# Kernel tuning notes

Hardware: AMD Instinct MI355X
Metric: run time of the kernel (lower is better)

## Reference

```python
import jax, jax.numpy as jnp
import numpy as np

N_SLICES = 2  # init kwarg n_slices


def affine_grid_3d(theta, D, H, W):
    """torch.nn.functional.affine_grid for 5D output, align_corners=False.
    theta: [B,3,4]; returns grid [B,D,H,W,3] with last dim (x,y,z) ~ (W,H,D)."""
    xs = (jnp.arange(W, dtype=theta.dtype) + 0.5) * (2.0 / W) - 1.0
    ys = (jnp.arange(H, dtype=theta.dtype) + 0.5) * (2.0 / H) - 1.0
    zs = (jnp.arange(D, dtype=theta.dtype) + 0.5) * (2.0 / D) - 1.0
    zz, yy, xx = jnp.meshgrid(zs, ys, xs, indexing='ij')
    base = jnp.stack([xx, yy, zz, jnp.ones_like(xx)], axis=-1)  # [D,H,W,4]
    return jnp.einsum('bij,dhwj->bdhwi', theta, base)  # [B,D,H,W,3]


def grid_sample_3d_zeros(vol, grid):
    """torch.nn.functional.grid_sample, mode='bilinear' (trilinear for 5D),
    padding_mode='zeros', align_corners=False.
    vol: [B,C,D,H,W]; grid: [B,D,H,W,3] normalized xyz coords."""
    B, C, D, H, W = vol.shape
    ix = ((grid[..., 0] + 1.0) * W - 1.0) * 0.5
    iy = ((grid[..., 1] + 1.0) * H - 1.0) * 0.5
    iz = ((grid[..., 2] + 1.0) * D - 1.0) * 0.5
    ix0 = jnp.floor(ix); iy0 = jnp.floor(iy); iz0 = jnp.floor(iz)
    fx = ix - ix0; fy = iy - iy0; fz = iz - iz0

    def gather(v, z, y, x):  # v: [C,D,H,W], idx: [D,H,W] -> [C,D,H,W]
        return v[:, z, y, x]

    out = jnp.zeros((B, C, D, H, W), vol.dtype)
    for dz in (0, 1):
        for dy in (0, 1):
            for dx in (0, 1):
                xi = ix0 + dx; yi = iy0 + dy; zi = iz0 + dz
                w = (jnp.where(dx, fx, 1.0 - fx)
                     * jnp.where(dy, fy, 1.0 - fy)
                     * jnp.where(dz, fz, 1.0 - fz))
                valid = ((xi >= 0) & (xi < W) & (yi >= 0) & (yi < H)
                         & (zi >= 0) & (zi < D))
                xc = jnp.clip(xi, 0, W - 1).astype(jnp.int32)
                yc = jnp.clip(yi, 0, H - 1).astype(jnp.int32)
                zc = jnp.clip(zi, 0, D - 1).astype(jnp.int32)
                vals = jax.vmap(gather)(vol, zc, yc, xc)  # [B,C,D,H,W]
                out = out + vals * (w * valid)[:, None]
    return out


def skip_connector(x, b_grid_affines):
    B, C, SPAT, _ = x.shape
    # zero volume with the 2D slice stack placed at the central W-plane
    vol = jnp.zeros((B, C, SPAT, SPAT, SPAT), x.dtype).at[..., SPAT // 2].set(x)
    chunks = jnp.split(vol, N_SLICES, axis=1)
    outs = []
    for i in range(N_SLICES):
        aff = b_grid_affines[i].astype(jnp.float32)  # [B,4,4]
        # get_zooms: column norms of rotation block
        zooms = jnp.sqrt((aff[:, :3, :3] ** 2).sum(axis=1))  # [B,3]
        # rescale_rot_components_with_diag(aff, 1/zooms) == aff @ diag(1/zx,1/zy,1/zz,1)
        scale = jnp.concatenate([1.0 / zooms, jnp.ones((aff.shape[0], 1), aff.dtype)], axis=1)
        aff = aff * scale[:, None, :]
        theta = jnp.linalg.inv(aff)[:, :3, :]  # [B,3,4]
        grid = affine_grid_3d(theta, SPAT, SPAT, SPAT)
        outs.append(grid_sample_3d_zeros(chunks[i], grid))
    return jnp.concatenate(outs, axis=1)  # [B,C,SPAT,SPAT,SPAT]


def setup_inputs() -> dict:
    key = jax.random.key(0)
    k1, k2 = jax.random.split(key)
    B, C, SPAT = 2, 32, 96
    x = jax.random.normal(k1, (B, C, SPAT, SPAT), dtype=jnp.float32)
    # near-identity invertible homogeneous affines for the two views (SA, HLA)
    noise = 0.1 * jax.random.normal(k2, (2, B, 4, 4), dtype=jnp.float32)
    aff = jnp.eye(4, dtype=jnp.float32)[None, None] + noise
    aff = aff.at[..., 3, :].set(jnp.array([0.0, 0.0, 0.0, 1.0], dtype=jnp.float32))
    return {"x": x, "b_grid_affines": aff}


def reference(x, b_grid_affines):
    return skip_connector(x, b_grid_affines)
```

## Files before the change

### kernel.cpp

```cpp
#include <hip/hip_runtime.h>
#include <math.h>

#define SPAT 96
#define PLANE (SPAT*SPAT*SPAT)
#define IMG   (SPAT*SPAT)

__device__ inline void invert4(const float m[16], float inv[16]) {
    inv[0]  =  m[5]*m[10]*m[15] - m[5]*m[11]*m[14] - m[9]*m[6]*m[15] + m[9]*m[7]*m[14] + m[13]*m[6]*m[11] - m[13]*m[7]*m[10];
    inv[4]  = -m[4]*m[10]*m[15] + m[4]*m[11]*m[14] + m[8]*m[6]*m[15] - m[8]*m[7]*m[14] - m[12]*m[6]*m[11] + m[12]*m[7]*m[10];
    inv[8]  =  m[4]*m[9]*m[15]  - m[4]*m[11]*m[13] - m[8]*m[5]*m[15] + m[8]*m[7]*m[13] + m[12]*m[5]*m[11] - m[12]*m[7]*m[9];
    inv[12] = -m[4]*m[9]*m[14]  + m[4]*m[10]*m[13] + m[8]*m[5]*m[14] - m[8]*m[6]*m[13] - m[12]*m[5]*m[10] + m[12]*m[6]*m[9];
    inv[1]  = -m[1]*m[10]*m[15] + m[1]*m[11]*m[14] + m[9]*m[2]*m[15] - m[9]*m[3]*m[14] - m[13]*m[2]*m[11] + m[13]*m[3]*m[10];
    inv[5]  =  m[0]*m[10]*m[15] - m[0]*m[11]*m[14] - m[8]*m[2]*m[15] + m[8]*m[3]*m[14] + m[12]*m[2]*m[11] - m[12]*m[3]*m[10];
    inv[9]  = -m[0]*m[9]*m[15]  + m[0]*m[11]*m[13] + m[8]*m[1]*m[15] - m[8]*m[3]*m[13] - m[12]*m[1]*m[11] + m[12]*m[3]*m[9];
    inv[13] =  m[0]*m[9]*m[14]  - m[0]*m[10]*m[13] - m[8]*m[1]*m[14] + m[8]*m[2]*m[13] + m[12]*m[1]*m[10] - m[12]*m[2]*m[9];
    inv[2]  =  m[1]*m[6]*m[15]  - m[1]*m[7]*m[14]  - m[5]*m[2]*m[15] + m[5]*m[3]*m[14] + m[13]*m[2]*m[7]  - m[13]*m[3]*m[6];
    inv[6]  = -m[0]*m[6]*m[15]  + m[0]*m[7]*m[14]  + m[4]*m[2]*m[15] - m[4]*m[3]*m[14] - m[12]*m[2]*m[7]  + m[12]*m[3]*m[6];
    inv[10] =  m[0]*m[5]*m[15]  - m[0]*m[7]*m[13]  - m[4]*m[1]*m[15] + m[4]*m[3]*m[13] + m[12]*m[1]*m[7]  - m[12]*m[3]*m[5];
    inv[14] = -m[0]*m[5]*m[14]  + m[0]*m[6]*m[13]  + m[4]*m[1]*m[14] - m[4]*m[2]*m[13] - m[12]*m[1]*m[6]  + m[12]*m[2]*m[5];
    inv[3]  = -m[1]*m[6]*m[11]  + m[1]*m[7]*m[10]  + m[5]*m[2]*m[11] - m[5]*m[3]*m[10] - m[9]*m[2]*m[7]   + m[9]*m[3]*m[6];
    inv[7]  =  m[0]*m[6]*m[11]  - m[0]*m[7]*m[10]  - m[4]*m[2]*m[11] + m[4]*m[3]*m[10] + m[8]*m[2]*m[7]   - m[8]*m[3]*m[6];
    inv[11] = -m[0]*m[5]*m[11]  + m[0]*m[7]*m[9]   + m[4]*m[1]*m[11] - m[4]*m[3]*m[9]  - m[8]*m[1]*m[7]   + m[8]*m[3]*m[5];
    inv[15] =  m[0]*m[5]*m[10]  - m[0]*m[6]*m[9]   - m[4]*m[1]*m[10] + m[4]*m[2]*m[9]  + m[8]*m[1]*m[6]   - m[8]*m[2]*m[5];
    float det  = m[0]*inv[0] + m[1]*inv[4] + m[2]*inv[8] + m[3]*inv[12];
    float rdet = 1.0f / det;
    for (int i = 0; i < 16; ++i) inv[i] *= rdet;
}

__global__ void prep_kernel(const float* __restrict__ aff_in,
                            float* __restrict__ Mout) {
    int t = threadIdx.x;
    if (t >= 4) return;
    float A[16];
    #pragma unroll
    for (int i = 0; i < 16; ++i) A[i] = aff_in[t * 16 + i];
    #pragma unroll
    for (int j = 0; j < 3; ++j) {
        float z = sqrtf(A[0*4+j]*A[0*4+j] + A[1*4+j]*A[1*4+j] + A[2*4+j]*A[2*4+j]);
        float rz = 1.0f / z;
        #pragma unroll
        for (int i = 0; i < 4; ++i) A[i*4+j] *= rz;
    }
    float inv[16];
    invert4(A, inv);
    float* M = Mout + t * 12;
    #pragma unroll
    for (int r = 0; r < 3; ++r) {
        float T0 = inv[r*4+0], T1 = inv[r*4+1], T2 = inv[r*4+2], T3 = inv[r*4+3];
        M[r*4+0] = T0;
        M[r*4+1] = T1;
        M[r*4+2] = T2;
        M[r*4+3] = -47.5f * (T0 + T1 + T2) + 48.0f * T3 + 47.5f;
    }
}

__global__ __launch_bounds__(256) void sample_kernel(
        const float* __restrict__ xin,
        const float* __restrict__ Mw,
        float* __restrict__ out) {
    int tf = blockIdx.x * 256 + threadIdx.x;
    int w4 = tf % 24;
    int h  = tf / 24;
    int d  = blockIdx.y;
    int sb = blockIdx.z;
    int s  = sb >> 1;
    int b  = sb & 1;

    const float* M = Mw + sb * 12;
    float Mxw = M[0], Mxh = M[1], Mxd = M[2],  Mx0 = M[3];
    float Myw = M[4], Myh = M[5], Myd = M[6],  My0 = M[7];
    float Mzw = M[8], Mzh = M[9], Mzd = M[10], Mz0 = M[11];

    float fh = (float)h, fd = (float)d;
    float bx = Mxh * fh + Mxd * fd + Mx0;
    float by = Myh * fh + Myd * fd + My0;
    float bz = Mzh * fh + Mzd * fd + Mz0;

    int w0 = w4 * 4;
    float wgt[4][4];
    int   off[4][4];
    bool  any = false;

    #pragma unroll
    for (int j = 0; j < 4; ++j) {
        float fw = (float)(w0 + j);
        float ix = Mxw * fw + bx;
        float iy = Myw * fw + by;
        float iz = Mzw * fw + bz;
        float wx = 1.0f - fabsf(ix - 48.0f);

        float w00 = 0.f, w01 = 0.f, w10 = 0.f, w11 = 0.f;
        int   o00 = 0,   o01 = 0,   o10 = 0,   o11 = 0;
        if (wx > 0.0f) {
            any = true;
            float yf = floorf(iy), zf = floorf(iz);
            float fy = iy - yf,    fz = iz - zf;
            int y0 = (int)yf, z0 = (int)zf;
            bool vy0 = (y0 >= 0)  & (y0 <  SPAT);
            bool vy1 = (y0 >= -1) & (y0 <  SPAT - 1);
            bool vz0 = (z0 >= 0)  & (z0 <  SPAT);
            bool vz1 = (z0 >= -1) & (z0 <  SPAT - 1);
            int y0c = min(max(y0, 0),     SPAT - 1);
            int y1c = min(max(y0 + 1, 0), SPAT - 1);
            int z0c = min(max(z0, 0),     SPAT - 1);
            int z1c = min(max(z0 + 1, 0), SPAT - 1);
            float wy0 = 1.0f - fy, wy1 = fy;
            float wz0 = 1.0f - fz, wz1 = fz;
            w00 = wx * wz0 * wy0 * ((vz0 & vy0) ? 1.0f : 0.0f);
            w01 = wx * wz0 * wy1 * ((vz0 & vy1) ? 1.0f : 0.0f);
            w10 = wx * wz1 * wy0 * ((vz1 & vy0) ? 1.0f : 0.0f);
            w11 = wx * wz1 * wy1 * ((vz1 & vy1) ? 1.0f : 0.0f);
            o00 = z0c * SPAT + y0c;  o01 = z0c * SPAT + y1c;
            o10 = z1c * SPAT + y0c;  o11 = z1c * SPAT + y1c;
        }
        wgt[j][0] = w00; wgt[j][1] = w01; wgt[j][2] = w10; wgt[j][3] = w11;
        off[j][0] = o00; off[j][1] = o01; off[j][2] = o10; off[j][3] = o11;
    }

    size_t cbase = (size_t)(b * 32 + s * 16);
    float* op = out + cbase * (size_t)PLANE + ((size_t)d * SPAT + h) * SPAT + w0;

    if (!any) {
        float4 z4 = make_float4(0.f, 0.f, 0.f, 0.f);
        #pragma unroll
        for (int c = 0; c < 16; ++c)
            *reinterpret_cast<float4*>(op + (size_t)c * PLANE) = z4;
    } else {
        const float* img = xin + cbase * (size_t)IMG;
        #pragma unroll
        for (int c = 0; c < 16; ++c) {
            const float* ic = img + (size_t)c * IMG;
            float r[4];
            #pragma unroll
            for (int j = 0; j < 4; ++j) {
                r[j] = wgt[j][0] * ic[off[j][0]] + wgt[j][1] * ic[off[j][1]]
                     + wgt[j][2] * ic[off[j][2]] + wgt[j][3] * ic[off[j][3]];
            }
            *reinterpret_cast<float4*>(op + (size_t)c * PLANE) =
                make_float4(r[0], r[1], r[2], r[3]);
        }
    }
}

extern "C" void kernel_launch(void* const* d_in, const int* in_sizes, int n_in,
                              void* d_out, int out_size, void* d_ws, size_t ws_size,
                              hipStream_t stream) {
    const float* x   = (const float*)d_in[0];
    const float* aff = (const float*)d_in[1];
    float* out = (float*)d_out;
    float* M   = (float*)d_ws;

    prep_kernel<<<1, 64, 0, stream>>>(aff, M);

    dim3 grid(9, SPAT, 4);
    sample_kernel<<<grid, 256, 0, stream>>>(x, M, out);
}
```

Baseline: 257.7 us.

## Zero output with bulk memset kernel and sample only the nonzero slab per row

A grid-stride zero kernel now clears the whole output. A new slab kernel then handles each (d,h) row and a group of 4 channels, solving analytically for the w-range where the x-tent weight is nonzero and writing only those voxels. The matrix prep moves into the slab kernel, computed by thread 0 into shared memory, which removes the separate prep launch. The cost is that every output byte is written once by the memset and the slab is written again, and the slab stores become scalar, strided across threads by row, instead of coalesced float4 stores.

```diff
diff --git a/kernel.cpp b/kernel.cpp
--- a/kernel.cpp
+++ b/kernel.cpp
@@ -4,6 +4,7 @@
 #define SPAT 96
 #define PLANE (SPAT*SPAT*SPAT)
 #define IMG   (SPAT*SPAT)
+#define OUT_FLOATS (64 * PLANE)
 
 __device__ inline void invert4(const float m[16], float inv[16]) {
     inv[0]  =  m[5]*m[10]*m[15] - m[5]*m[11]*m[14] - m[9]*m[6]*m[15] + m[9]*m[7]*m[14] + m[13]*m[6]*m[11] - m[13]*m[7]*m[10];
@@ -27,117 +28,115 @@
     for (int i = 0; i < 16; ++i) inv[i] *= rdet;
 }
 
-__global__ void prep_kernel(const float* __restrict__ aff_in,
-                            float* __restrict__ Mout) {
-    int t = threadIdx.x;
-    if (t >= 4) return;
-    float A[16];
-    #pragma unroll
-    for (int i = 0; i < 16; ++i) A[i] = aff_in[t * 16 + i];
-    #pragma unroll
-    for (int j = 0; j < 3; ++j) {
-        float z = sqrtf(A[0*4+j]*A[0*4+j] + A[1*4+j]*A[1*4+j] + A[2*4+j]*A[2*4+j]);
-        float rz = 1.0f / z;
-        #pragma unroll
-        for (int i = 0; i < 4; ++i) A[i*4+j] *= rz;
-    }
-    float inv[16];
-    invert4(A, inv);
-    float* M = Mout + t * 12;
-    #pragma unroll
-    for (int r = 0; r < 3; ++r) {
-        float T0 = inv[r*4+0], T1 = inv[r*4+1], T2 = inv[r*4+2], T3 = inv[r*4+3];
-        M[r*4+0] = T0;
-        M[r*4+1] = T1;
-        M[r*4+2] = T2;
-        M[r*4+3] = -47.5f * (T0 + T1 + T2) + 48.0f * T3 + 47.5f;
-    }
+__global__ __launch_bounds__(256) void zero_kernel(float4* __restrict__ out) {
+    const size_t n4 = OUT_FLOATS / 4;
+    size_t i = (size_t)blockIdx.x * 256 + threadIdx.x;
+    size_t stride = (size_t)gridDim.x * 256;
+    float4 z = make_float4(0.f, 0.f, 0.f, 0.f);
+    for (; i < n4; i += stride) out[i] = z;
 }
 
-__global__ __launch_bounds__(256) void sample_kernel(
+__global__ __launch_bounds__(256) void slab_kernel(
         const float* __restrict__ xin,
-        const float* __restrict__ Mw,
+        const float* __restrict__ aff_in,
         float* __restrict__ out) {
-    int tf = blockIdx.x * 256 + threadIdx.x;
-    int w4 = tf % 24;
-    int h  = tf / 24;
-    int d  = blockIdx.y;
-    int sb = blockIdx.z;
+    __shared__ float Ms[12];
+    int sb = blockIdx.y;
+    if (threadIdx.x == 0) {
+        float A[16];
+        #pragma unroll
+        for (int i = 0; i < 16; ++i) A[i] = aff_in[sb * 16 + i];
+        #pragma unroll
+        for (int j = 0; j < 3; ++j) {
+            float z = sqrtf(A[0*4+j]*A[0*4+j] + A[1*4+j]*A[1*4+j] + A[2*4+j]*A[2*4+j]);
+            float rz = 1.0f / z;
+            #pragma unroll
+            for (int i = 0; i < 4; ++i) A[i*4+j] *= rz;
+        }
+        float inv[16];
+        invert4(A, inv);
+        #pragma unroll
+        for (int r = 0; r < 3; ++r) {
+            float T0 = inv[r*4+0], T1 = inv[r*4+1], T2 = inv[r*4+2], T3 = inv[r*4+3];
+            Ms[r*4+0] = T0;
+            Ms[r*4+1] = T1;
+            Ms[r*4+2] = T2;
+            Ms[r*4+3] = -47.5f * (T0 + T1 + T2) + 48.0f * T3 + 47.5f;
+        }
+    }
+    __syncthreads();
+
+    int t  = blockIdx.x * 256 + threadIdx.x;
+    int cg = t & 3;
+    int hd = t >> 2;
+    int h  = hd % SPAT;
+    int d  = hd / SPAT;
     int s  = sb >> 1;
     int b  = sb & 1;
 
-    const float* M = Mw + sb * 12;
-    float Mxw = M[0], Mxh = M[1], Mxd = M[2],  Mx0 = M[3];
-    float Myw = M[4], Myh = M[5], Myd = M[6],  My0 = M[7];
-    float Mzw = M[8], Mzh = M[9], Mzd = M[10], Mz0 = M[11];
+    float Mxw = Ms[0], Mxh = Ms[1], Mxd = Ms[2],  Mx0 = Ms[3];
+    float Myw = Ms[4], Myh = Ms[5], Myd = Ms[6],  My0 = Ms[7];
+    float Mzw = Ms[8], Mzh = Ms[9], Mzd = Ms[10], Mz0 = Ms[11];
 
     float fh = (float)h, fd = (float)d;
     float bx = Mxh * fh + Mxd * fd + Mx0;
     float by = Myh * fh + Myd * fd + My0;
     float bz = Mzh * fh + Mzd * fd + Mz0;
 
-    int w0 = w4 * 4;
-    float wgt[4][4];
-    int   off[4][4];
-    bool  any = false;
+    int wlo, whi;
+    if (fabsf(Mxw) > 1e-6f) {
+        float w1 = (47.0f - bx) / Mxw;
+        float w2 = (49.0f - bx) / Mxw;
+        float wmin = fminf(w1, w2), wmax = fmaxf(w1, w2);
+        wlo = (int)ceilf(wmin);
+        whi = (int)floorf(wmax);
+        wlo = max(wlo, 0);
+        whi = min(whi, SPAT - 1);
+    } else {
+        bool in = fabsf(bx - 48.0f) < 1.0f;
+        wlo = in ? 0 : 1;
+        whi = in ? SPAT - 1 : 0;
+    }
+    if (wlo > whi) return;
 
-    #pragma unroll
-    for (int j = 0; j < 4; ++j) {
-        float fw = (float)(w0 + j);
+    size_t cbase = (size_t)(b * 32 + s * 16 + cg * 4);
+    const float* img = xin + cbase * (size_t)IMG;
+    float* op = out + cbase * (size_t)PLANE + ((size_t)d * SPAT + h) * SPAT;
+
+    for (int w = wlo; w <= whi; ++w) {
+        float fw = (float)w;
         float ix = Mxw * fw + bx;
+        float wx = 1.0f - fabsf(ix - 48.0f);
+        if (wx <= 0.0f) continue;
         float iy = Myw * fw + by;
         float iz = Mzw * fw + bz;
-        float wx = 1.0f - fabsf(ix - 48.0f);
 
-        float w00 = 0.f, w01 = 0.f, w10 = 0.f, w11 = 0.f;
-        int   o00 = 0,   o01 = 0,   o10 = 0,   o11 = 0;
-        if (wx > 0.0f) {
-            any = true;
-            float yf = floorf(iy), zf = floorf(iz);
-            float fy = iy - yf,    fz = iz - zf;
-            int y0 = (int)yf, z0 = (int)zf;
-            bool vy0 = (y0 >= 0)  & (y0 <  SPAT);
-            bool vy1 = (y0 >= -1) & (y0 <  SPAT - 1);
-            bool vz0 = (z0 >= 0)  & (z0 <  SPAT);
-            bool vz1 = (z0 >= -1) & (z0 <  SPAT - 1);
-            int y0c = min(max(y0, 0),     SPAT - 1);
-            int y1c = min(max(y0 + 1, 0), SPAT - 1);
-            int z0c = min(max(z0, 0),     SPAT - 1);
-            int z1c = min(max(z0 + 1, 0), SPAT - 1);
-            float wy0 = 1.0f - fy, wy1 = fy;
-            float wz0 = 1.0f - fz, wz1 = fz;
-            w00 = wx * wz0 * wy0 * ((vz0 & vy0) ? 1.0f : 0.0f);
-            w01 = wx * wz0 * wy1 * ((vz0 & vy1) ? 1.0f : 0.0f);
-            w10 = wx * wz1 * wy0 * ((vz1 & vy0) ? 1.0f : 0.0f);
-            w11 = wx * wz1 * wy1 * ((vz1 & vy1) ? 1.0f : 0.0f);
-            o00 = z0c * SPAT + y0c;  o01 = z0c * SPAT + y1c;
-            o10 = z1c * SPAT + y0c;  o11 = z1c * SPAT + y1c;
-        }
-        wgt[j][0] = w00; wgt[j][1] = w01; wgt[j][2] = w10; wgt[j][3] = w11;
-        off[j][0] = o00; off[j][1] = o01; off[j][2] = o10; off[j][3] = o11;
-    }
+        float yf = floorf(iy), zf = floorf(iz);
+        float fy = iy - yf,    fz = iz - zf;
+        int y0 = (int)yf, z0 = (int)zf;
+        bool vy0 = (y0 >= 0)  & (y0 <  SPAT);
+        bool vy1 = (y0 >= -1) & (y0 <  SPAT - 1);
+        bool vz0 = (z0 >= 0)  & (z0 <  SPAT);
+        bool vz1 = (z0 >= -1) & (z0 <  SPAT - 1);
+        int y0c = min(max(y0, 0),     SPAT - 1);
+        int y1c = min(max(y0 + 1, 0), SPAT - 1);
+        int z0c = min(max(z0, 0),     SPAT - 1);
+        int z1c = min(max(z0 + 1, 0), SPAT - 1);
+        float wy0 = 1.0f - fy, wy1 = fy;
+        float wz0 = 1.0f - fz, wz1 = fz;
+        float w00 = wx * wz0 * wy0 * ((vz0 & vy0) ? 1.0f : 0.0f);
+        float w01 = wx * wz0 * wy1 * ((vz0 & vy1) ? 1.0f : 0.0f);
+        float w10 = wx * wz1 * wy0 * ((vz1 & vy0) ? 1.0f : 0.0f);
+        float w11 = wx * wz1 * wy1 * ((vz1 & vy1) ? 1.0f : 0.0f);
+        int o00 = z0c * SPAT + y0c, o01 = z0c * SPAT + y1c;
+        int o10 = z1c * SPAT + y0c, o11 = z1c * SPAT + y1c;
 
-    size_t cbase = (size_t)(b * 32 + s * 16);
-    float* op = out + cbase * (size_t)PLANE + ((size_t)d * SPAT + h) * SPAT + w0;
-
-    if (!any) {
-        float4 z4 = make_float4(0.f, 0.f, 0.f, 0.f);
         #pragma unroll
-        for (int c = 0; c < 16; ++c)
-            *reinterpret_cast<float4*>(op + (size_t)c * PLANE) = z4;
-    } else {
-        const float* img = xin + cbase * (size_t)IMG;
-        #pragma unroll
-        for (int c = 0; c < 16; ++c) {
+        for (int c = 0; c < 4; ++c) {
             const float* ic = img + (size_t)c * IMG;
-            float r[4];
-            #pragma unroll
-            for (int j = 0; j < 4; ++j) {
-                r[j] = wgt[j][0] * ic[off[j][0]] + wgt[j][1] * ic[off[j][1]]
-                     + wgt[j][2] * ic[off[j][2]] + wgt[j][3] * ic[off[j][3]];
-            }
-            *reinterpret_cast<float4*>(op + (size_t)c * PLANE) =
-                make_float4(r[0], r[1], r[2], r[3]);
+            float r = w00 * ic[o00] + w01 * ic[o01]
+                    + w10 * ic[o10] + w11 * ic[o11];
+            op[(size_t)c * PLANE + w] = r;
         }
     }
 }
@@ -148,10 +147,9 @@
     const float* x   = (const float*)d_in[0];
     const float* aff = (const float*)d_in[1];
     float* out = (float*)d_out;
-    float* M   = (float*)d_ws;
 
-    prep_kernel<<<1, 64, 0, stream>>>(aff, M);
+    zero_kernel<<<4096, 256, 0, stream>>>((float4*)out);
 
-    dim3 grid(9, SPAT, 4);
-    sample_kernel<<<grid, 256, 0, stream>>>(x, M, out);
+    dim3 grid(144, 4);
+    slab_kernel<<<grid, 256, 0, stream>>>(x, aff, out);
 }
```

After: 243.0 us. -5.7%, faster.

## Split sampling into analytic slab-interval compute blocks and separate zero-fill blocks

Applied to the files above, without the earlier changes.

Computes per-(d,h) row the analytic W interval where the x-weight is nonzero, using a precomputed reciprocal of Mxw. Compute blocks then sample only the float4 groups inside that interval, with 4 channels per thread. Separate zero-fill blocks write plain float4 zeros to every other position. This removes per-element weight evaluation and branch divergence across the mostly-zero output, and spreads the writes over more blocks. The cost is extra index maths, and the interval boundaries must match exactly so no element is missed or written twice.

```diff
diff --git a/kernel.cpp b/kernel.cpp
--- a/kernel.cpp
+++ b/kernel.cpp
@@ -4,6 +4,9 @@
 #define SPAT 96
 #define PLANE (SPAT*SPAT*SPAT)
 #define IMG   (SPAT*SPAT)
+#define NCHUNK (64 * SPAT * SPAT * 24)
+#define ZBLOCKS (NCHUNK / 256)
+#define SLAB_BLOCKS 576
 
 __device__ inline void invert4(const float m[16], float inv[16]) {
     inv[0]  =  m[5]*m[10]*m[15] - m[5]*m[11]*m[14] - m[9]*m[6]*m[15] + m[9]*m[7]*m[14] + m[13]*m[6]*m[11] - m[13]*m[7]*m[10];
@@ -43,7 +46,7 @@
     }
     float inv[16];
     invert4(A, inv);
-    float* M = Mout + t * 12;
+    float* M = Mout + t * 16;
     #pragma unroll
     for (int r = 0; r < 3; ++r) {
         float T0 = inv[r*4+0], T1 = inv[r*4+1], T2 = inv[r*4+2], T3 = inv[r*4+3];
@@ -52,92 +55,132 @@
         M[r*4+2] = T2;
         M[r*4+3] = -47.5f * (T0 + T1 + T2) + 48.0f * T3 + 47.5f;
     }
+    float Mxw = M[0];
+    M[12] = (fabsf(Mxw) > 1e-6f) ? (1.0f / Mxw) : 0.0f;
+    M[13] = 0.f; M[14] = 0.f; M[15] = 0.f;
 }
 
-__global__ __launch_bounds__(256) void sample_kernel(
+__device__ inline void w_interval(float Mxw, float rMxw, float bx,
+                                  int& wlo, int& whi) {
+    if (fabsf(Mxw) > 1e-6f) {
+        float w1 = (47.0f - bx) * rMxw;
+        float w2 = (49.0f - bx) * rMxw;
+        float wmin = fminf(w1, w2), wmax = fmaxf(w1, w2);
+        wlo = max((int)ceilf(wmin), 0);
+        whi = min((int)floorf(wmax), SPAT - 1);
+    } else {
+        bool in = fabsf(bx - 48.0f) < 1.0f;
+        wlo = in ? 0 : 1;
+        whi = in ? SPAT - 1 : 0;
+    }
+}
+
+__global__ __launch_bounds__(256) void fused_kernel(
         const float* __restrict__ xin,
         const float* __restrict__ Mw,
         float* __restrict__ out) {
-    int tf = blockIdx.x * 256 + threadIdx.x;
-    int w4 = tf % 24;
-    int h  = tf / 24;
-    int d  = blockIdx.y;
-    int sb = blockIdx.z;
-    int s  = sb >> 1;
-    int b  = sb & 1;
+    int bid = blockIdx.x;
+    if (bid < SLAB_BLOCKS) {
+        int sb  = bid / 144;
+        int rem = bid - sb * 144;
+        int t   = rem * 256 + threadIdx.x;
+        int cg  = t & 3;
+        int hd  = t >> 2;
+        int h   = hd % SPAT;
+        int d   = hd / SPAT;
+        int s   = sb >> 1;
+        int b   = sb & 1;
 
-    const float* M = Mw + sb * 12;
-    float Mxw = M[0], Mxh = M[1], Mxd = M[2],  Mx0 = M[3];
-    float Myw = M[4], Myh = M[5], Myd = M[6],  My0 = M[7];
-    float Mzw = M[8], Mzh = M[9], Mzd = M[10], Mz0 = M[11];
+        const float* M = Mw + sb * 16;
+        float Mxw = M[0], Mxh = M[1], Mxd = M[2],  Mx0 = M[3];
+        float Myw = M[4], Myh = M[5], Myd = M[6],  My0 = M[7];
+        float Mzw = M[8], Mzh = M[9], Mzd = M[10], Mz0 = M[11];
+        float rMxw = M[12];
 
-    float fh = (float)h, fd = (float)d;
-    float bx = Mxh * fh + Mxd * fd + Mx0;
-    float by = Myh * fh + Myd * fd + My0;
-    float bz = Mzh * fh + Mzd * fd + Mz0;
+        float fh = (float)h, fd = (float)d;
+        float bx = Mxh * fh + Mxd * fd + Mx0;
+        int wlo, whi;
+        w_interval(Mxw, rMxw, bx, wlo, whi);
+        if (wlo > whi) return;
+        int qlo = wlo >> 2, qhi = whi >> 2;
 
-    int w0 = w4 * 4;
-    float wgt[4][4];
-    int   off[4][4];
-    bool  any = false;
+        float by = Myh * fh + Myd * fd + My0;
+        float bz = Mzh * fh + Mzd * fd + Mz0;
 
-    #pragma unroll
-    for (int j = 0; j < 4; ++j) {
-        float fw = (float)(w0 + j);
-        float ix = Mxw * fw + bx;
-        float iy = Myw * fw + by;
-        float iz = Mzw * fw + bz;
-        float wx = 1.0f - fabsf(ix - 48.0f);
+        size_t cbase = (size_t)(b * 32 + s * 16 + cg * 4);
+        const float* img = xin + cbase * (size_t)IMG;
+        float* op = out + cbase * (size_t)PLANE + ((size_t)d * SPAT + h) * SPAT;
 
-        float w00 = 0.f, w01 = 0.f, w10 = 0.f, w11 = 0.f;
-        int   o00 = 0,   o01 = 0,   o10 = 0,   o11 = 0;
-        if (wx > 0.0f) {
-            any = true;
-            float yf = floorf(iy), zf = floorf(iz);
-            float fy = iy - yf,    fz = iz - zf;
-            int y0 = (int)yf, z0 = (int)zf;
-            bool vy0 = (y0 >= 0)  & (y0 <  SPAT);
-            bool vy1 = (y0 >= -1) & (y0 <  SPAT - 1);
-            bool vz0 = (z0 >= 0)  & (z0 <  SPAT);
-            bool vz1 = (z0 >= -1) & (z0 <  SPAT - 1);
-            int y0c = min(max(y0, 0),     SPAT - 1);
-            int y1c = min(max(y0 + 1, 0), SPAT - 1);
-            int z0c = min(max(z0, 0),     SPAT - 1);
-            int z1c = min(max(z0 + 1, 0), SPAT - 1);
-            float wy0 = 1.0f - fy, wy1 = fy;
-            float wz0 = 1.0f - fz, wz1 = fz;
-            w00 = wx * wz0 * wy0 * ((vz0 & vy0) ? 1.0f : 0.0f);
-            w01 = wx * wz0 * wy1 * ((vz0 & vy1) ? 1.0f : 0.0f);
-            w10 = wx * wz1 * wy0 * ((vz1 & vy0) ? 1.0f : 0.0f);
-            w11 = wx * wz1 * wy1 * ((vz1 & vy1) ? 1.0f : 0.0f);
-            o00 = z0c * SPAT + y0c;  o01 = z0c * SPAT + y1c;
-            o10 = z1c * SPAT + y0c;  o11 = z1c * SPAT + y1c;
-        }
-        wgt[j][0] = w00; wgt[j][1] = w01; wgt[j][2] = w10; wgt[j][3] = w11;
-        off[j][0] = o00; off[j][1] = o01; off[j][2] = o10; off[j][3] = o11;
-    }
-
-    size_t cbase = (size_t)(b * 32 + s * 16);
-    float* op = out + cbase * (size_t)PLANE + ((size_t)d * SPAT + h) * SPAT + w0;
-
-    if (!any) {
-        float4 z4 = make_float4(0.f, 0.f, 0.f, 0.f);
-        #pragma unroll
-        for (int c = 0; c < 16; ++c)
-            *reinterpret_cast<float4*>(op + (size_t)c * PLANE) = z4;
-    } else {
-        const float* img = xin + cbase * (size_t)IMG;
-        #pragma unroll
-        for (int c = 0; c < 16; ++c) {
-            const float* ic = img + (size_t)c * IMG;
-            float r[4];
+        for (int q = qlo; q <= qhi; ++q) {
+            float v[4][4];
             #pragma unroll
             for (int j = 0; j < 4; ++j) {
-                r[j] = wgt[j][0] * ic[off[j][0]] + wgt[j][1] * ic[off[j][1]]
-                     + wgt[j][2] * ic[off[j][2]] + wgt[j][3] * ic[off[j][3]];
+                float fw = (float)(4 * q + j);
+                float ix = Mxw * fw + bx;
+                float wx = 1.0f - fabsf(ix - 48.0f);
+                if (wx > 0.0f) {
+                    float iy = Myw * fw + by;
+                    float iz = Mzw * fw + bz;
+                    float yf = floorf(iy), zf = floorf(iz);
+                    float fy = iy - yf,    fz = iz - zf;
+                    int y0 = (int)yf, z0 = (int)zf;
+                    bool vy0 = (y0 >= 0)  & (y0 <  SPAT);
+                    bool vy1 = (y0 >= -1) & (y0 <  SPAT - 1);
+                    bool vz0 = (z0 >= 0)  & (z0 <  SPAT);
+                    bool vz1 = (z0 >= -1) & (z0 <  SPAT - 1);
+                    int y0c = min(max(y0, 0),     SPAT - 1);
+                    int y1c = min(max(y0 + 1, 0), SPAT - 1);
+                    int z0c = min(max(z0, 0),     SPAT - 1);
+                    int z1c = min(max(z0 + 1, 0), SPAT - 1);
+                    float wy0 = 1.0f - fy, wy1 = fy;
+                    float wz0 = 1.0f - fz, wz1 = fz;
+                    float w00 = wx * wz0 * wy0 * ((vz0 & vy0) ? 1.0f : 0.0f);
+                    float w01 = wx * wz0 * wy1 * ((vz0 & vy1) ? 1.0f : 0.0f);
+                    float w10 = wx * wz1 * wy0 * ((vz1 & vy0) ? 1.0f : 0.0f);
+                    float w11 = wx * wz1 * wy1 * ((vz1 & vy1) ? 1.0f : 0.0f);
+                    int o00 = z0c * SPAT + y0c, o01 = z0c * SPAT + y1c;
+                    int o10 = z1c * SPAT + y0c, o11 = z1c * SPAT + y1c;
+                    #pragma unroll
+                    for (int c = 0; c < 4; ++c) {
+                        const float* ic = img + (size_t)c * IMG;
+                        v[c][j] = w00 * ic[o00] + w01 * ic[o01]
+                                + w10 * ic[o10] + w11 * ic[o11];
+                    }
+                } else {
+                    #pragma unroll
+                    for (int c = 0; c < 4; ++c) v[c][j] = 0.0f;
+                }
             }
-            *reinterpret_cast<float4*>(op + (size_t)c * PLANE) =
-                make_float4(r[0], r[1], r[2], r[3]);
+            #pragma unroll
+            for (int c = 0; c < 4; ++c) {
+                *reinterpret_cast<float4*>(op + (size_t)c * PLANE + 4 * q) =
+                    make_float4(v[c][0], v[c][1], v[c][2], v[c][3]);
+            }
+        }
+    } else {
+        int g  = (bid - SLAB_BLOCKS) * 256 + threadIdx.x;
+        int w4 = g % 24;
+        int r1 = g / 24;
+        int h  = r1 % SPAT;
+        int r2 = r1 / SPAT;
+        int d  = r2 % SPAT;
+        int c  = r2 / SPAT;
+        int b  = c >> 5;
+        int s  = (c >> 4) & 1;
+        int sb = s * 2 + b;
+
+        const float* M = Mw + sb * 16;
+        float Mxw = M[0], Mxh = M[1], Mxd = M[2], Mx0 = M[3];
+        float rMxw = M[12];
+
+        float bx = Mxh * (float)h + Mxd * (float)d + Mx0;
+        int wlo, whi;
+        w_interval(Mxw, rMxw, bx, wlo, whi);
+        bool owned_by_slab = (wlo <= whi) && (w4 >= (wlo >> 2)) && (w4 <= (whi >> 2));
+        if (!owned_by_slab) {
+            float4 z = make_float4(0.f, 0.f, 0.f, 0.f);
+            *reinterpret_cast<float4*>(
+                out + (size_t)c * PLANE + ((size_t)d * SPAT + h) * SPAT + 4 * w4) = z;
         }
     }
 }
@@ -151,7 +194,5 @@
     float* M   = (float*)d_ws;
 
     prep_kernel<<<1, 64, 0, stream>>>(aff, M);
-
-    dim3 grid(9, SPAT, 4);
-    sample_kernel<<<grid, 256, 0, stream>>>(x, M, out);
+    fused_kernel<<<SLAB_BLOCKS + ZBLOCKS, 256, 0, stream>>>(x, M, out);
 }
```

New measurement: 251.9 us. -2.3%, faster.
